# Optimization experiments

Measured on AMD Instinct MI355X. Metric: run time of the kernel, lower is better.

The kernel has to match this reference:

```python
import jax, jax.numpy as jnp
import numpy as np

B, C_FEAT, C_CODE, H, W = 32, 768, 70, 28, 28
FS = 11
NEG = 5
POS_INTRA_SHIFT = 0.18
POS_INTER_SHIFT = 0.12
NEG_INTER_SHIFT = 0.46


def _norm(t):
    # F.normalize(t, dim=1, eps=1e-10)
    n = jnp.sqrt(jnp.sum(t * t, axis=1, keepdims=True))
    return t / jnp.maximum(n, 1e-10)


def _grid_sample(t, coords):
    # torch: F.grid_sample(t, coords.permute(0,2,1,3), padding_mode='border', align_corners=True)
    grid = jnp.transpose(coords, (0, 2, 1, 3))  # [N, Hg, Wg, 2], last dim = (x, y)
    N, C, Hi, Wi = t.shape
    # align_corners=True unnormalize, then border-clip the continuous coordinate
    x = jnp.clip((grid[..., 0] + 1.0) * 0.5 * (Wi - 1), 0.0, Wi - 1.0)
    y = jnp.clip((grid[..., 1] + 1.0) * 0.5 * (Hi - 1), 0.0, Hi - 1.0)
    x0 = jnp.floor(x)
    y0 = jnp.floor(y)
    wx = (x - x0)[:, None]  # broadcast over channel dim
    wy = (y - y0)[:, None]
    x0i = x0.astype(jnp.int32)
    y0i = y0.astype(jnp.int32)
    x1i = jnp.minimum(x0i + 1, Wi - 1)
    y1i = jnp.minimum(y0i + 1, Hi - 1)
    gather = jax.vmap(lambda img, yi, xi: img[:, yi, xi])  # [C,Hg,Wg] per batch elem
    v00 = gather(t, y0i, x0i)
    v01 = gather(t, y0i, x1i)
    v10 = gather(t, y1i, x0i)
    v11 = gather(t, y1i, x1i)
    return (v00 * (1.0 - wx) * (1.0 - wy) + v01 * wx * (1.0 - wy)
            + v10 * (1.0 - wx) * wy + v11 * wx * wy)


def _helper(f1, f2, c1, c2, shift):
    # fd under torch.no_grad -> stop_gradient
    fd = jnp.einsum('nchw,ncij->nhwij', _norm(f1), _norm(f2))
    old_mean = fd.mean()  # pointwise=True branch
    fd = fd - fd.mean(axis=(3, 4), keepdims=True)
    fd = jax.lax.stop_gradient(fd - fd.mean() + old_mean)
    cd = jnp.einsum('nchw,ncij->nhwij', _norm(c1), _norm(c2))
    # zero_clamp=True -> min_val=0.0; stabalize=True -> clamp max 0.8
    loss = -jnp.clip(cd, 0.0, 0.8) * (fd - shift)
    return loss, cd


def _forward(orig_feats, orig_feats_pos, orig_code, orig_code_pos,
             depth_aug_feats, depth_aug_feats_pos, coords1, coords2, perms):
    c1 = coords1 * 2.0 - 1.0
    c2 = coords2 * 2.0 - 1.0
    feats = _grid_sample(orig_feats, c1)
    code = _grid_sample(orig_code, c1)
    feats_pos = _grid_sample(orig_feats_pos, c2)
    code_pos = _grid_sample(orig_code_pos, c2)
    daf = _grid_sample(depth_aug_feats, c1)
    _ = _grid_sample(depth_aug_feats_pos, c2)  # computed (as in torch) but unused

    pos_intra_loss, pos_intra_cd = _helper(daf, daf, code, code, POS_INTRA_SHIFT)
    pos_inter_loss, pos_inter_cd = _helper(feats, feats_pos, code, code_pos, POS_INTER_SHIFT)

    neg_losses, neg_cds = [], []
    for i in range(perms.shape[0]):  # fixed small neg_samples loop
        p = perms[i]
        feats_neg = _grid_sample(orig_feats[p], c2)
        code_neg = _grid_sample(orig_code[p], c2)
        l, cd = _helper(feats, feats_neg, code, code_neg, NEG_INTER_SHIFT)
        neg_losses.append(l)
        neg_cds.append(cd)
    neg_inter_loss = jnp.concatenate(neg_losses, axis=0)
    neg_inter_cd = jnp.concatenate(neg_cds, axis=0)
    return (pos_intra_loss.mean(), pos_intra_cd,
            pos_inter_loss.mean(), pos_inter_cd,
            neg_inter_loss, neg_inter_cd)


def setup_inputs() -> dict:
    key = jax.random.key(0)
    ks = jax.random.split(key, 10)
    rng = np.random.default_rng(0)
    perms = []
    for _ in range(NEG):  # super_perm: derangement-ish permutation
        p = rng.permutation(B)
        p = np.where(p == np.arange(B), p + 1, p) % B
        perms.append(p)
    return {
        'orig_feats': jax.random.normal(ks[0], (B, C_FEAT, H, W), jnp.float32),
        'orig_feats_pos': jax.random.normal(ks[1], (B, C_FEAT, H, W), jnp.float32),
        'orig_salience': jnp.zeros((B, H, W), jnp.float32),
        'orig_salience_pos': jnp.zeros((B, H, W), jnp.float32),
        'orig_code': jax.random.normal(ks[2], (B, C_CODE, H, W), jnp.float32),
        'orig_code_pos': jax.random.normal(ks[3], (B, C_CODE, H, W), jnp.float32),
        'depth_aug_feats': jax.random.normal(ks[4], (B, C_FEAT, H, W), jnp.float32),
        'depth_aug_feats_pos': jax.random.normal(ks[5], (B, C_FEAT, H, W), jnp.float32),
        'coords1': jax.random.uniform(ks[6], (B, FS, FS, 2), jnp.float32),
        'coords2': jax.random.uniform(ks[7], (B, FS, FS, 2), jnp.float32),
        'perms': jnp.asarray(np.stack(perms), dtype=jnp.int32),
    }


def reference(orig_feats, orig_feats_pos, orig_salience, orig_salience_pos,
              orig_code, orig_code_pos, depth_aug_feats, depth_aug_feats_pos,
              coords1, coords2, perms):
    # use_salience=False: salience tensors unused
    return _forward(orig_feats, orig_feats_pos, orig_code, orig_code_pos,
                    depth_aug_feats, depth_aug_feats_pos, coords1, coords2, perms)
```

## Files before the change

### kernel.cpp

```cpp
#include <hip/hip_runtime.h>

#define CF 768
#define CCODE 70
#define NPIX 784
#define P 121
#define NB 32
#define NTOTF 468512.0f

#define OFF_PI_SCALAR 0
#define OFF_PI_CD 1
#define OFF_PO_SCALAR 468513
#define OFF_PO_CD 468514
#define OFF_NEG_LOSS 937026
#define OFF_NEG_CD 3279586

#define WS_BSUMS 0
#define WS_ADDT 1536
#define WS_NSQF 2048
#define WS_NSQC 395264
#define WS_FRAG_FLOAT 423936
#define FEAT_FRAG_SHORTS 98304
#define CODE_FRAG_SHORTS 12288
#define FEATS_TOTAL_SHORTS (8 * 32 * FEAT_FRAG_SHORTS)
#define CODE_BASE_SHORTS FEATS_TOTAL_SHORTS
#define CODE_TOTAL_SHORTS (7 * 32 * CODE_FRAG_SHORTS)
#define WS_NEED2 (WS_FRAG_FLOAT + (FEATS_TOTAL_SHORTS + CODE_TOTAL_SHORTS) / 2)

typedef __attribute__((ext_vector_type(8))) short short8;
typedef __attribute__((ext_vector_type(4))) float f32x4;
typedef unsigned short ushort_t;
typedef unsigned int uint_t;

__device__ __forceinline__ float samp4(const float* __restrict__ img, int c,
                                       const int4 o, const float4 w) {
  const float* p = img + c * NPIX;
  return w.x * p[o.x] + w.y * p[o.y] + w.z * p[o.z] + w.w * p[o.w];
}

__device__ __forceinline__ void mkcoord(const float* cp, int4* o, float4* w) {
  float x = fminf(fmaxf(cp[0] * 27.f, 0.f), 27.f);
  float y = fminf(fmaxf(cp[1] * 27.f, 0.f), 27.f);
  float x0f = floorf(x), y0f = floorf(y);
  int x0 = (int)x0f, y0 = (int)y0f;
  int x1 = min(x0 + 1, 27), y1 = min(y0 + 1, 27);
  float wx = x - x0f, wy = y - y0f;
  *o = make_int4(y0 * 28 + x0, y0 * 28 + x1, y1 * 28 + x0, y1 * 28 + x1);
  *w = make_float4((1.f - wx) * (1.f - wy), wx * (1.f - wy),
                   (1.f - wx) * wy, wx * wy);
}

__device__ __forceinline__ void mkcoord2(const float* cp, int2* o, float4* w) {
  float x = fminf(fmaxf(cp[0] * 27.f, 0.f), 27.f);
  float y = fminf(fmaxf(cp[1] * 27.f, 0.f), 27.f);
  float x0f = floorf(x), y0f = floorf(y);
  int x0 = (int)x0f, y0 = (int)y0f;
  int y1 = min(y0 + 1, 27);
  float wx = x - x0f, wy = y - y0f;
  bool sh = (x0 >= 27);
  int xb = sh ? 26 : x0;
  float wa0 = sh ? 0.f : (1.f - wx) * (1.f - wy);
  float wa1 = sh ? (1.f - wy) : wx * (1.f - wy);
  float wb0 = sh ? 0.f : (1.f - wx) * wy;
  float wb1 = sh ? wy : wx * wy;
  *o = make_int2(y0 * 28 + xb, y1 * 28 + xb);
  *w = make_float4(wa0, wa1, wb0, wb1);
}

__device__ __forceinline__ ushort_t f2bf(float x) {
  uint_t u = __float_as_uint(x);
  u += 0x7fffu + ((u >> 16) & 1u);
  return (ushort_t)(u >> 16);
}

__global__ __launch_bounds__(256) void presample_fz(
    const float* __restrict__ OF, const float* __restrict__ OFP,
    const float* __restrict__ OC, const float* __restrict__ OCP,
    const float* __restrict__ DAF,
    const float* __restrict__ CO1, const float* __restrict__ CO2,
    const int* __restrict__ PERMS, float* __restrict__ ws) {
  ushort_t* frags = (ushort_t*)(ws + WS_FRAG_FLOAT);
  __shared__ float planes[8 * NPIX];
  __shared__ int sh_slot[16], sh_n[16], sh_cb[16];
  __shared__ int sh_ncs;
  const int job = (int)(((long long)blockIdx.x * 405) % 1216);
  const int tid = threadIdx.x;

  int tensor, m, g0, G;
  if (job < 384) { tensor = 0; m = job / 12; g0 = (job - m * 12) * 8; G = 8; }
  else if (job < 768) { int j = job - 384; tensor = 1; m = j / 12; g0 = (j - m * 12) * 8; G = 8; }
  else if (job < 1152) { int j = job - 768; tensor = 2; m = j / 12; g0 = (j - m * 12) * 8; G = 8; }
  else if (job < 1184) { tensor = 3; m = job - 1152; g0 = 0; G = 12; }
  else { tensor = 4; m = job - 1184; g0 = 0; G = 12; }

  const float* src;
  int nch;
  bool feat;
  if (tensor == 0) { src = OF + (size_t)m * CF * NPIX; nch = CF; feat = true; }
  else if (tensor == 1) { src = DAF + (size_t)m * CF * NPIX; nch = CF; feat = true; }
  else if (tensor == 2) { src = OFP + (size_t)m * CF * NPIX; nch = CF; feat = true; }
  else if (tensor == 3) { src = OC + (size_t)m * CCODE * NPIX; nch = CCODE; feat = false; }
  else { src = OCP + (size_t)m * CCODE * NPIX; nch = CCODE; feat = false; }

  if (tid == 0) {
    int cnt = 0;
    if (tensor == 0) {
      sh_slot[0] = 1; sh_n[0] = m; sh_cb[0] = 0; cnt = 1;
      for (int i = 0; i < 5; ++i)
        for (int k = 0; k < NB; ++k)
          if (PERMS[i * NB + k] == m) {
            sh_slot[cnt] = 3 + i; sh_n[cnt] = k; sh_cb[cnt] = 1; ++cnt;
          }
    } else if (tensor == 1) { sh_slot[0] = 0; sh_n[0] = m; sh_cb[0] = 0; cnt = 1; }
    else if (tensor == 2) { sh_slot[0] = 2; sh_n[0] = m; sh_cb[0] = 1; cnt = 1; }
    else if (tensor == 3) {
      sh_slot[0] = 0; sh_n[0] = m; sh_cb[0] = 0; cnt = 1;
      for (int i = 0; i < 5; ++i)
        for (int k = 0; k < NB; ++k)
          if (PERMS[i * NB + k] == m) {
            sh_slot[cnt] = 2 + i; sh_n[cnt] = k; sh_cb[cnt] = 1; ++cnt;
          }
    } else { sh_slot[0] = 1; sh_n[0] = m; sh_cb[0] = 1; cnt = 1; }
    sh_ncs = cnt;
  }

  float4 buf0, buf1, buf2, buf3, buf4, buf5, buf6;
#define LOAD_OCT(OCT)                                                        \
  {                                                                          \
    const int c0_ = (OCT) * 8;                                               \
    int valid_ = nch - c0_;                                                  \
    valid_ = valid_ > 8 ? 8 : (valid_ < 0 ? 0 : valid_);                     \
    const int lim4_ = valid_ * (NPIX / 4);                                   \
    const float4* sc_ = (const float4*)(src + (size_t)c0_ * NPIX);           \
    int e_;                                                                  \
    e_ = tid;          buf0 = (e_ < lim4_) ? sc_[e_] : make_float4(0,0,0,0); \
    e_ = tid + 256;    buf1 = (e_ < lim4_) ? sc_[e_] : make_float4(0,0,0,0); \
    e_ = tid + 512;    buf2 = (e_ < lim4_) ? sc_[e_] : make_float4(0,0,0,0); \
    e_ = tid + 768;    buf3 = (e_ < lim4_) ? sc_[e_] : make_float4(0,0,0,0); \
    e_ = tid + 1024;   buf4 = (e_ < lim4_) ? sc_[e_] : make_float4(0,0,0,0); \
    e_ = tid + 1280;   buf5 = (e_ < lim4_) ? sc_[e_] : make_float4(0,0,0,0); \
    e_ = tid + 1536;                                                         \
    buf6 = (e_ < 1568 && e_ < lim4_) ? sc_[e_] : make_float4(0,0,0,0);       \
  }

  LOAD_OCT(g0);
  __syncthreads();

  const int total = sh_ncs * 128;
  const int sub = g0 >> 3;
  int2 o_0, o_1, o_2, o_3, o_4, o_5;
  float4 w_0, w_1, w_2, w_3, w_4, w_5;
  uint_t b_0 = 0, b_1 = 0, b_2 = 0, b_3 = 0, b_4 = 0, b_5 = 0;
  uint_t nq_0 = 0, nq_1 = 0, nq_2 = 0, nq_3 = 0, nq_4 = 0, nq_5 = 0;
  float sq_0 = 0.f, sq_1 = 0.f, sq_2 = 0.f, sq_3 = 0.f, sq_4 = 0.f, sq_5 = 0.f;
#define SETUP_SLOT(J, OV, WV, BV, NQV)                                       \
  {                                                                          \
    const int s_ = tid + (J) * 256;                                          \
    OV = make_int2(0, 0);                                                    \
    WV = make_float4(0.f, 0.f, 0.f, 0.f);                                    \
    if (s_ < total) {                                                        \
      const int cs_ = s_ >> 7, pt_ = s_ & 127;                               \
      const int slot_ = sh_slot[cs_], n_ = sh_n[cs_];                        \
      const float* cb_ = sh_cb[cs_] ? CO2 : CO1;                             \
      size_t fb_ = feat ? (size_t)(slot_ * 32 + n_) * FEAT_FRAG_SHORTS       \
                        : CODE_BASE_SHORTS +                                 \
                              (size_t)(slot_ * 32 + n_) * CODE_FRAG_SHORTS;  \
      BV = (uint_t)(fb_ + ((size_t)((pt_ >> 4) * 64 + (pt_ & 15)) << 3));    \
      NQV = feat ? (uint_t)(WS_NSQF +                                        \
                            ((slot_ * 32 + n_) * 12 + sub) * 128 + pt_)      \
                 : (uint_t)(WS_NSQC + (slot_ * 32 + n_) * 128 + pt_);        \
      if (pt_ < P) {                                                         \
        int gi_ = pt_ / 11, gj_ = pt_ - gi_ * 11;                            \
        mkcoord2(cb_ + (((n_ * 11 + gj_) * 11 + gi_) << 1), &OV, &WV);       \
      }                                                                      \
    }                                                                        \
  }
  SETUP_SLOT(0, o_0, w_0, b_0, nq_0)
  SETUP_SLOT(1, o_1, w_1, b_1, nq_1)
  SETUP_SLOT(2, o_2, w_2, b_2, nq_2)
  SETUP_SLOT(3, o_3, w_3, b_3, nq_3)
  SETUP_SLOT(4, o_4, w_4, b_4, nq_4)
  SETUP_SLOT(5, o_5, w_5, b_5, nq_5)
#undef SETUP_SLOT

#define DO_SLOT(J, OV, WV, BV, SQV)                                          \
  if (tid + (J) * 256 < total) {                                             \
    float v_[8];                                                             \
    _Pragma("unroll") for (int i_ = 0; i_ < 8; ++i_) {                       \
      const float* pl_ = planes + i_ * NPIX;                                 \
      v_[i_] = WV.x * pl_[OV.x] + WV.y * pl_[OV.x + 1] +                     \
               WV.z * pl_[OV.y] + WV.w * pl_[OV.y + 1];                      \
      SQV = fmaf(v_[i_], v_[i_], SQV);                                       \
    }                                                                        \
    uint4 q_;                                                                \
    q_.x = (uint_t)f2bf(v_[0]) | ((uint_t)f2bf(v_[1]) << 16);                \
    q_.y = (uint_t)f2bf(v_[2]) | ((uint_t)f2bf(v_[3]) << 16);                \
    q_.z = (uint_t)f2bf(v_[4]) | ((uint_t)f2bf(v_[5]) << 16);                \
    q_.w = (uint_t)f2bf(v_[6]) | ((uint_t)f2bf(v_[7]) << 16);                \
    *(uint4*)(frags + BV + octoff) = q_;                                     \
  }

  for (int g = 0; g < G; ++g) {
    const int o = g0 + g;
    if (g) __syncthreads();
    {
      float4* pl4 = (float4*)planes;
      int e;
      e = tid;        pl4[e] = buf0;
      e = tid + 256;  pl4[e] = buf1;
      e = tid + 512;  pl4[e] = buf2;
      e = tid + 768;  pl4[e] = buf3;
      e = tid + 1024; pl4[e] = buf4;
      e = tid + 1280; pl4[e] = buf5;
      e = tid + 1536; if (e < 1568) pl4[e] = buf6;
    }
    __syncthreads();
    if (g + 1 < G) LOAD_OCT(g0 + g + 1);

    const uint_t octoff = (uint_t)((o >> 2) * 4096 + (o & 3) * 128);
    DO_SLOT(0, o_0, w_0, b_0, sq_0)
    DO_SLOT(1, o_1, w_1, b_1, sq_1)
    DO_SLOT(2, o_2, w_2, b_2, sq_2)
    DO_SLOT(3, o_3, w_3, b_3, sq_3)
    DO_SLOT(4, o_4, w_4, b_4, sq_4)
    DO_SLOT(5, o_5, w_5, b_5, sq_5)
  }
#undef DO_SLOT
#undef LOAD_OCT

  if (tid < total) ws[nq_0] = sq_0;
  if (tid + 256 < total) ws[nq_1] = sq_1;
  if (tid + 512 < total) ws[nq_2] = sq_2;
  if (tid + 768 < total) ws[nq_3] = sq_3;
  if (tid + 1024 < total) ws[nq_4] = sq_4;
  if (tid + 1280 < total) ws[nq_5] = sq_5;
}

__global__ __launch_bounds__(256) void gram_mfma2(float* __restrict__ ws,
                                                  float* __restrict__ out) {
  const ushort_t* frags = (const ushort_t*)(ws + WS_FRAG_FLOAT);
  const int bid = blockIdx.x;
  const int half = bid & 1, pairn = bid >> 1;
  const int pair = pairn >> 5, n = pairn & 31;
  const int tid = threadIdx.x, wave = tid >> 6, lane = tid & 63;
  __shared__ float invAf[128], invBf[128], invAc[128], invBc[128];
  __shared__ float red[4][3];
  const int afslot = (pair == 0) ? 0 : 1;
  const int bfslot = (pair == 0) ? 0 : (pair == 1 ? 2 : 3 + (pair - 2));
  const int bcslot = (pair == 0) ? 0 : (pair == 1 ? 1 : 2 + (pair - 2));
  if (tid < 128) {
    float s;
    const float* p;
    p = ws + WS_NSQF + (size_t)(afslot * 32 + n) * 12 * 128 + tid;
    s = 0.f;
#pragma unroll
    for (int u = 0; u < 12; ++u) s += p[u * 128];
    invAf[tid] = 1.f / fmaxf(sqrtf(s), 1e-10f);
    p = ws + WS_NSQF + (size_t)(bfslot * 32 + n) * 12 * 128 + tid;
    s = 0.f;
#pragma unroll
    for (int u = 0; u < 12; ++u) s += p[u * 128];
    invBf[tid] = 1.f / fmaxf(sqrtf(s), 1e-10f);
    invAc[tid] = 1.f / fmaxf(sqrtf(ws[WS_NSQC + (0 * 32 + n) * 128 + tid]), 1e-10f);
    invBc[tid] = 1.f / fmaxf(sqrtf(ws[WS_NSQC + (bcslot * 32 + n) * 128 + tid]), 1e-10f);
  }
  __syncthreads();

  const short8* Af = (const short8*)(frags + (size_t)(afslot * 32 + n) * FEAT_FRAG_SHORTS);
  const short8* Bf = (const short8*)(frags + (size_t)(bfslot * 32 + n) * FEAT_FRAG_SHORTS);
  const int rt = half * 4 + wave;

  f32x4 acc[8];
#pragma unroll
  for (int t = 0; t < 8; ++t) acc[t] = (f32x4){0.f, 0.f, 0.f, 0.f};

#pragma unroll 2
  for (int kp = 0; kp < 24; ++kp) {
    short8 a0 = Af[(kp * 8 + rt) * 64 + lane];
    short8 bv[8];
#pragma unroll
    for (int t = 0; t < 8; ++t) bv[t] = Bf[(kp * 8 + t) * 64 + lane];
#pragma unroll
    for (int t = 0; t < 8; ++t)
      acc[t] = __builtin_amdgcn_mfma_f32_16x16x32_bf16(a0, bv[t], acc[t], 0, 0, 0);
  }

  const int lane4 = (lane >> 4) << 2;
  const int cl15 = lane & 15;
  const int rb = rt * 16 + lane4;
  float sfd = 0.f;
  {
    const float ivr0 = invAf[rb], ivr1 = invAf[rb + 1], ivr2 = invAf[rb + 2],
                ivr3 = invAf[rb + 3];
    float rs0 = 0.f, rs1 = 0.f, rs2 = 0.f, rs3 = 0.f;
#pragma unroll
    for (int t = 0; t < 8; ++t) {
      const float ivc = invBf[t * 16 + cl15];
      float v0 = acc[t].x * ivr0 * ivc;
      float v1 = acc[t].y * ivr1 * ivc;
      float v2 = acc[t].z * ivr2 * ivc;
      float v3 = acc[t].w * ivr3 * ivc;
      acc[t].x = v0; acc[t].y = v1; acc[t].z = v2; acc[t].w = v3;
      rs0 += v0; rs1 += v1; rs2 += v2; rs3 += v3;
    }
    sfd = rs0 + rs1 + rs2 + rs3;
    rs0 += __shfl_xor(rs0, 1); rs0 += __shfl_xor(rs0, 2);
    rs0 += __shfl_xor(rs0, 4); rs0 += __shfl_xor(rs0, 8);
    rs1 += __shfl_xor(rs1, 1); rs1 += __shfl_xor(rs1, 2);
    rs1 += __shfl_xor(rs1, 4); rs1 += __shfl_xor(rs1, 8);
    rs2 += __shfl_xor(rs2, 1); rs2 += __shfl_xor(rs2, 2);
    rs2 += __shfl_xor(rs2, 4); rs2 += __shfl_xor(rs2, 8);
    rs3 += __shfl_xor(rs3, 1); rs3 += __shfl_xor(rs3, 2);
    rs3 += __shfl_xor(rs3, 4); rs3 += __shfl_xor(rs3, 8);
    const float rm0 = rs0 * (1.f / 121.f), rm1 = rs1 * (1.f / 121.f);
    const float rm2 = rs2 * (1.f / 121.f), rm3 = rs3 * (1.f / 121.f);
#pragma unroll
    for (int t = 0; t < 8; ++t) {
      acc[t].x -= rm0; acc[t].y -= rm1; acc[t].z -= rm2; acc[t].w -= rm3;
    }
  }

  int cd_base, loss_base = 0;
  if (pair == 0) cd_base = OFF_PI_CD + n * 14641;
  else if (pair == 1) cd_base = OFF_PO_CD + n * 14641;
  else {
    int t0 = ((pair - 2) * NB + n) * 14641;
    cd_base = OFF_NEG_CD + t0;
    loss_base = OFF_NEG_LOSS + t0;
  }

  if (pair >= 2 && rb < P) {
#pragma unroll
    for (int t = 0; t < 8; ++t) {
      const int c = t * 16 + cl15;
      if (c < P) {
        float* o = out + loss_base + rb * P + c;
        o[0] = acc[t].x;
        if (rb + 1 < P) o[P] = acc[t].y;
        if (rb + 2 < P) o[2 * P] = acc[t].z;
        if (rb + 3 < P) o[3 * P] = acc[t].w;
      }
    }
  }

  const short8* Ac = (const short8*)(frags + CODE_BASE_SHORTS + (size_t)n * CODE_FRAG_SHORTS);
  const short8* Bc = (const short8*)(frags + CODE_BASE_SHORTS + (size_t)(bcslot * 32 + n) * CODE_FRAG_SHORTS);
  f32x4 cacc[8];
#pragma unroll
  for (int t = 0; t < 8; ++t) cacc[t] = (f32x4){0.f, 0.f, 0.f, 0.f};
#pragma unroll
  for (int kp = 0; kp < 3; ++kp) {
    short8 a0 = Ac[(kp * 8 + rt) * 64 + lane];
    short8 bv[8];
#pragma unroll
    for (int t = 0; t < 8; ++t) bv[t] = Bc[(kp * 8 + t) * 64 + lane];
#pragma unroll
    for (int t = 0; t < 8; ++t)
      cacc[t] = __builtin_amdgcn_mfma_f32_16x16x32_bf16(a0, bv[t], cacc[t], 0, 0, 0);
  }

  float s1 = 0.f, s2 = 0.f;
  {
    const float ivr0 = invAc[rb], ivr1 = invAc[rb + 1], ivr2 = invAc[rb + 2],
                ivr3 = invAc[rb + 3];
#pragma unroll
    for (int t = 0; t < 8; ++t) {
      const int c = t * 16 + cl15;
      const float ivc = invBc[c];
      float c0v = cacc[t].x * ivr0 * ivc;
      float c1v = cacc[t].y * ivr1 * ivc;
      float c2v = cacc[t].z * ivr2 * ivc;
      float c3v = cacc[t].w * ivr3 * ivc;
      if (c < P && rb < P) {
        float* o = out + cd_base + rb * P + c;
        o[0] = c0v;
        if (rb + 1 < P) o[P] = c1v;
        if (rb + 2 < P) o[2 * P] = c2v;
        if (rb + 3 < P) o[3 * P] = c3v;
      }
      if (pair < 2) {
        float cl0 = fminf(fmaxf(c0v, 0.f), 0.8f);
        float cl1 = fminf(fmaxf(c1v, 0.f), 0.8f);
        float cl2 = fminf(fmaxf(c2v, 0.f), 0.8f);
        float cl3 = fminf(fmaxf(c3v, 0.f), 0.8f);
        s1 = fmaf(cl0, acc[t].x, s1);
        s1 = fmaf(cl1, acc[t].y, s1);
        s1 = fmaf(cl2, acc[t].z, s1);
        s1 = fmaf(cl3, acc[t].w, s1);
        s2 += cl0 + cl1 + cl2 + cl3;
      }
    }
  }

#pragma unroll
  for (int m = 1; m < 64; m <<= 1) {
    sfd += __shfl_xor(sfd, m);
    s1 += __shfl_xor(s1, m);
    s2 += __shfl_xor(s2, m);
  }
  if ((tid & 63) == 0) { red[wave][0] = sfd; red[wave][1] = s1; red[wave][2] = s2; }
  __syncthreads();
  if (tid == 0) {
    float a = 0.f, b2 = 0.f, c2 = 0.f;
    for (int w = 0; w < 4; ++w) { a += red[w][0]; b2 += red[w][1]; c2 += red[w][2]; }
    float* bsums = ws + WS_BSUMS;
    bsums[bid * 3 + 0] = a;
    bsums[bid * 3 + 1] = b2;
    bsums[bid * 3 + 2] = c2;
  }
}

__global__ void loss_finish3(float* __restrict__ ws, float* __restrict__ out) {
  __shared__ float s[7][3];
  const float* bsums = ws + WS_BSUMS;
  float* addterm = ws + WS_ADDT;
  int tid = threadIdx.x;
  if (tid < 21) {
    int pr = tid / 3, k = tid % 3;
    float a = 0.f;
    for (int i = 0; i < 64; ++i) a += bsums[(pr * 64 + i) * 3 + k];
    s[pr][k] = a;
  }
  __syncthreads();
  if (tid == 0) {
    const float invN = 1.f / NTOTF;
    out[OFF_PI_SCALAR] = -(s[0][1] + (s[0][0] * invN - 0.18f) * s[0][2]) * invN;
    out[OFF_PO_SCALAR] = -(s[1][1] + (s[1][0] * invN - 0.12f) * s[1][2]) * invN;
  }
  if (tid >= 1 && tid < 6) addterm[tid - 1] = s[tid + 1][0] / NTOTF - 0.46f;
}

__global__ __launch_bounds__(256) void neg_loss_kernel(
    float* __restrict__ lossr, const float* __restrict__ cdr,
    const float* __restrict__ addterm) {
  __shared__ float at[5];
  if (threadIdx.x < 5) at[threadIdx.x] = addterm[threadIdx.x];
  __syncthreads();
  const int total4 = 5 * 117128;
  float4* l4 = (float4*)lossr;
  const float4* c4 = (const float4*)cdr;
  for (int e = blockIdx.x * 256 + threadIdx.x; e < total4; e += gridDim.x * 256) {
    int k = e / 117128;
    float4 cd = c4[e];
    float4 fv = l4[e];
    float a = at[k];
    float4 r;
    r.x = -fminf(fmaxf(cd.x, 0.f), 0.8f) * (fv.x + a);
    r.y = -fminf(fmaxf(cd.y, 0.f), 0.8f) * (fv.y + a);
    r.z = -fminf(fmaxf(cd.z, 0.f), 0.8f) * (fv.z + a);
    r.w = -fminf(fmaxf(cd.w, 0.f), 0.8f) * (fv.w + a);
    l4[e] = r;
  }
}


__global__ __launch_bounds__(256) void loss_main_fb(
    const float* __restrict__ OF, const float* __restrict__ OFP,
    const float* __restrict__ OC, const float* __restrict__ OCP,
    const float* __restrict__ DAF,
    const float* __restrict__ CO1, const float* __restrict__ CO2,
    const int* __restrict__ PERMS,
    float* __restrict__ out, float* __restrict__ bsums) {
  const int b = blockIdx.x;
  const int pair = b >> 7;
  const int rem = b & 127;
  const int n = rem >> 2;
  const int rg = rem & 3;
  const int row_start = rg * 31;
  const int rcount = min(31, P - row_start);
  const int tid = threadIdx.x;
  const int tx = tid & 15, ty = tid >> 4;

  const float *F1, *F2, *C1, *C2, *CB;
  if (pair == 0) {
    F1 = DAF + (size_t)n * CF * NPIX; F2 = F1;
    C1 = OC + (size_t)n * CCODE * NPIX; C2 = C1;
    CB = CO1;
  } else if (pair == 1) {
    F1 = OF + (size_t)n * CF * NPIX; F2 = OFP + (size_t)n * CF * NPIX;
    C1 = OC + (size_t)n * CCODE * NPIX; C2 = OCP + (size_t)n * CCODE * NPIX;
    CB = CO2;
  } else {
    int n2 = PERMS[(pair - 2) * NB + n];
    F1 = OF + (size_t)n * CF * NPIX; F2 = OF + (size_t)n2 * CF * NPIX;
    C1 = OC + (size_t)n * CCODE * NPIX; C2 = OC + (size_t)n2 * CCODE * NPIX;
    CB = CO2;
  }

  __shared__ int4 Bo[P];
  __shared__ float4 Bw[P];
  __shared__ int4 Ao[32];
  __shared__ float4 Aw[32];
  __shared__ float Abuf[CCODE][32];
  __shared__ float Bbuf[CCODE][128];
  __shared__ float invA[32], invB[128];
  __shared__ float red[4][3];

  if (tid < P) {
    int gi = tid / 11, gj = tid - gi * 11;
    const float* cp = CB + (((n * 11 + gj) * 11 + gi) << 1);
    mkcoord(cp, &Bo[tid], &Bw[tid]);
  } else if (tid >= 128 && tid < 160) {
    int r = tid - 128;
    int q = row_start + r;
    if (q < P) {
      int gi = q / 11, gj = q - gi * 11;
      const float* cp = CO1 + (((n * 11 + gj) * 11 + gi) << 1);
      mkcoord(cp, &Ao[r], &Aw[r]);
    }
  }
  __syncthreads();

  float acc[2][2][4];
#pragma unroll
  for (int kr = 0; kr < 2; ++kr)
#pragma unroll
    for (int m = 0; m < 2; ++m)
#pragma unroll
      for (int u = 0; u < 4; ++u) acc[kr][m][u] = 0.f;
  float ansq = 0.f, bnsq = 0.f;

  for (int ch = 0; ch < 12; ++ch) {
    const int c0 = ch * 64;
    if (ch) __syncthreads();
    for (int e = tid; e < 64 * 128; e += 256) {
      int col = e & 127, cc = e >> 7;
      float v = 0.f;
      if (col < P) v = samp4(F2, c0 + cc, Bo[col], Bw[col]);
      Bbuf[cc][col] = v;
    }
    for (int e = tid; e < 64 * 32; e += 256) {
      int col = e & 31, cc = e >> 5;
      float v = 0.f;
      if (col < rcount) v = samp4(F1, c0 + cc, Ao[col], Aw[col]);
      Abuf[cc][col] = v;
    }
    __syncthreads();
    if (tid < 128) {
      float s = 0.f;
      for (int cc = 0; cc < 64; ++cc) { float v = Bbuf[cc][tid]; s = fmaf(v, v, s); }
      bnsq += s;
    } else if (tid < 160) {
      int r = tid - 128;
      float s = 0.f;
      for (int cc = 0; cc < 64; ++cc) { float v = Abuf[cc][r]; s = fmaf(v, v, s); }
      ansq += s;
    }
    for (int cc = 0; cc < 64; ++cc) {
      const float2 av = *(const float2*)&Abuf[cc][ty * 2];
      const float4 b0 = *(const float4*)&Bbuf[cc][tx * 4];
      const float4 b1 = *(const float4*)&Bbuf[cc][tx * 4 + 64];
      float a[2] = {av.x, av.y};
      float bb[2][4] = {{b0.x, b0.y, b0.z, b0.w}, {b1.x, b1.y, b1.z, b1.w}};
#pragma unroll
      for (int kr = 0; kr < 2; ++kr)
#pragma unroll
        for (int m = 0; m < 2; ++m)
#pragma unroll
          for (int u = 0; u < 4; ++u)
            acc[kr][m][u] = fmaf(a[kr], bb[m][u], acc[kr][m][u]);
    }
  }
  __syncthreads();
  if (tid < 128) invB[tid] = (tid < P) ? 1.f / fmaxf(sqrtf(bnsq), 1e-10f) : 0.f;
  else if (tid < 160) {
    int r = tid - 128;
    invA[r] = (r < rcount) ? 1.f / fmaxf(sqrtf(ansq), 1e-10f) : 0.f;
  }
  __syncthreads();

  float ia[2] = {invA[2 * ty], invA[2 * ty + 1]};
  float ib[2][4];
#pragma unroll
  for (int m = 0; m < 2; ++m)
#pragma unroll
    for (int u = 0; u < 4; ++u) ib[m][u] = invB[m * 64 + tx * 4 + u];

  float fdc[2][2][4];
  float sfd = 0.f;
#pragma unroll
  for (int kr = 0; kr < 2; ++kr) {
    float part = 0.f;
#pragma unroll
    for (int m = 0; m < 2; ++m)
#pragma unroll
      for (int u = 0; u < 4; ++u) {
        float v = acc[kr][m][u] * ia[kr] * ib[m][u];
        fdc[kr][m][u] = v;
        part += v;
      }
    sfd += part;
    float rs = part;
#pragma unroll
    for (int s = 1; s < 16; s <<= 1) rs += __shfl_xor(rs, s, 16);
    float rowm = rs * (1.f / 121.f);
#pragma unroll
    for (int m = 0; m < 2; ++m)
#pragma unroll
      for (int u = 0; u < 4; ++u) fdc[kr][m][u] -= rowm;
  }
  __syncthreads();

  for (int e = tid; e < CCODE * 128; e += 256) {
    int col = e & 127, cc = e >> 7;
    float v = 0.f;
    if (col < P) v = samp4(C2, cc, Bo[col], Bw[col]);
    Bbuf[cc][col] = v;
  }
  for (int e = tid; e < CCODE * 32; e += 256) {
    int col = e & 31, cc = e >> 5;
    float v = 0.f;
    if (col < rcount) v = samp4(C1, cc, Ao[col], Aw[col]);
    Abuf[cc][col] = v;
  }
  __syncthreads();
  if (tid < 128) {
    float s = 0.f;
    for (int cc = 0; cc < CCODE; ++cc) { float v = Bbuf[cc][tid]; s = fmaf(v, v, s); }
    invB[tid] = (tid < P) ? 1.f / fmaxf(sqrtf(s), 1e-10f) : 0.f;
  } else if (tid < 160) {
    int r = tid - 128;
    float s = 0.f;
    for (int cc = 0; cc < CCODE; ++cc) { float v = Abuf[cc][r]; s = fmaf(v, v, s); }
    invA[r] = (r < rcount) ? 1.f / fmaxf(sqrtf(s), 1e-10f) : 0.f;
  }
  float cacc[2][2][4];
#pragma unroll
  for (int kr = 0; kr < 2; ++kr)
#pragma unroll
    for (int m = 0; m < 2; ++m)
#pragma unroll
      for (int u = 0; u < 4; ++u) cacc[kr][m][u] = 0.f;
  for (int cc = 0; cc < CCODE; ++cc) {
    const float2 av = *(const float2*)&Abuf[cc][ty * 2];
    const float4 b0 = *(const float4*)&Bbuf[cc][tx * 4];
    const float4 b1 = *(const float4*)&Bbuf[cc][tx * 4 + 64];
    float a[2] = {av.x, av.y};
    float bb[2][4] = {{b0.x, b0.y, b0.z, b0.w}, {b1.x, b1.y, b1.z, b1.w}};
#pragma unroll
    for (int kr = 0; kr < 2; ++kr)
#pragma unroll
      for (int m = 0; m < 2; ++m)
#pragma unroll
        for (int u = 0; u < 4; ++u)
          cacc[kr][m][u] = fmaf(a[kr], bb[m][u], cacc[kr][m][u]);
  }
  __syncthreads();
  float iac[2] = {invA[2 * ty], invA[2 * ty + 1]};
  float ibc[2][4];
#pragma unroll
  for (int m = 0; m < 2; ++m)
#pragma unroll
    for (int u = 0; u < 4; ++u) ibc[m][u] = invB[m * 64 + tx * 4 + u];

  int cd_base, loss_base = 0;
  if (pair == 0) cd_base = OFF_PI_CD + n * 14641;
  else if (pair == 1) cd_base = OFF_PO_CD + n * 14641;
  else {
    int t = ((pair - 2) * NB + n) * 14641;
    cd_base = OFF_NEG_CD + t;
    loss_base = OFF_NEG_LOSS + t;
  }

  float s1 = 0.f, s2 = 0.f;
#pragma unroll
  for (int kr = 0; kr < 2; ++kr) {
    int r = 2 * ty + kr;
    if (r < rcount) {
      int rglob = row_start + r;
#pragma unroll
      for (int m = 0; m < 2; ++m)
#pragma unroll
        for (int u = 0; u < 4; ++u) {
          int c = m * 64 + tx * 4 + u;
          if (c < P) {
            float cdv = cacc[kr][m][u] * iac[kr] * ibc[m][u];
            int idx = rglob * P + c;
            out[cd_base + idx] = cdv;
            float cl = fminf(fmaxf(cdv, 0.f), 0.8f);
            float fv = fdc[kr][m][u];
            if (pair < 2) { s1 = fmaf(cl, fv, s1); s2 += cl; }
            else out[loss_base + idx] = fv;
          }
        }
    }
  }

#pragma unroll
  for (int s = 1; s < 64; s <<= 1) {
    sfd += __shfl_xor(sfd, s);
    s1 += __shfl_xor(s1, s);
    s2 += __shfl_xor(s2, s);
  }
  int wv = tid >> 6;
  if ((tid & 63) == 0) { red[wv][0] = sfd; red[wv][1] = s1; red[wv][2] = s2; }
  __syncthreads();
  if (tid == 0) {
    float a = 0.f, bb = 0.f, cc = 0.f;
    for (int w = 0; w < 4; ++w) { a += red[w][0]; bb += red[w][1]; cc += red[w][2]; }
    bsums[b * 3 + 0] = a;
    bsums[b * 3 + 1] = bb;
    bsums[b * 3 + 2] = cc;
  }
}

__global__ void loss_finish_fb(const float* __restrict__ bsums,
                               float* __restrict__ out,
                               float* __restrict__ addterm) {
  __shared__ float s[7][3];
  int tid = threadIdx.x;
  if (tid < 21) {
    int pr = tid / 3, k = tid % 3;
    float a = 0.f;
    const float* p = bsums + (pr * 128) * 3 + k;
    for (int i = 0; i < 128; ++i) a += p[i * 3];
    s[pr][k] = a;
  }
  __syncthreads();
  if (tid == 0) {
    const float invN = 1.f / NTOTF;
    out[OFF_PI_SCALAR] = -(s[0][1] + (s[0][0] * invN - 0.18f) * s[0][2]) * invN;
    out[OFF_PO_SCALAR] = -(s[1][1] + (s[1][0] * invN - 0.12f) * s[1][2]) * invN;
  }
  if (tid >= 1 && tid < 6) addterm[tid - 1] = s[tid + 1][0] / NTOTF - 0.46f;
}

__global__ __launch_bounds__(256) void neg_loss_fb(
    float* __restrict__ lossr, const float* __restrict__ cdr,
    const float* __restrict__ addterm) {
  __shared__ float at[5];
  if (threadIdx.x < 5) at[threadIdx.x] = addterm[threadIdx.x];
  __syncthreads();
  const int total = 5 * 468512;
  for (int e = blockIdx.x * 256 + threadIdx.x; e < total; e += gridDim.x * 256) {
    int k = e / 468512;
    float cdv = cdr[e];
    float cl = fminf(fmaxf(cdv, 0.f), 0.8f);
    lossr[e] = -cl * (lossr[e] + at[k]);
  }
}

extern "C" void kernel_launch(void* const* d_in, const int* in_sizes, int n_in,
                              void* d_out, int out_size, void* d_ws,
                              size_t ws_size, hipStream_t stream) {
  const float* OF = (const float*)d_in[0];
  const float* OFP = (const float*)d_in[1];
  const float* OC = (const float*)d_in[4];
  const float* OCP = (const float*)d_in[5];
  const float* DAF = (const float*)d_in[6];
  const float* CO1 = (const float*)d_in[8];
  const float* CO2 = (const float*)d_in[9];
  const int* PERMS = (const int*)d_in[10];
  float* out = (float*)d_out;
  float* ws = (float*)d_ws;

  if (ws_size >= (size_t)WS_NEED2 * sizeof(float)) {
    hipLaunchKernelGGL(presample_fz, dim3(1216), dim3(256), 0, stream,
                       OF, OFP, OC, OCP, DAF, CO1, CO2, PERMS, ws);
    hipLaunchKernelGGL(gram_mfma2, dim3(448), dim3(256), 0, stream, ws, out);
    hipLaunchKernelGGL(loss_finish3, dim3(1), dim3(64), 0, stream, ws, out);
    hipLaunchKernelGGL(neg_loss_kernel, dim3(2048), dim3(256), 0, stream,
                       out + OFF_NEG_LOSS, out + OFF_NEG_CD, ws + WS_ADDT);
  } else {
    float* bsums = ws;
    float* addterm = bsums + 896 * 3;
    hipLaunchKernelGGL(loss_main_fb, dim3(896), dim3(256), 0, stream,
                       OF, OFP, OC, OCP, DAF, CO1, CO2, PERMS, out, bsums);
    hipLaunchKernelGGL(loss_finish_fb, dim3(1), dim3(64), 0, stream,
                       bsums, out, addterm);
    hipLaunchKernelGGL(neg_loss_fb, dim3(2048), dim3(256), 0, stream,
                       out + OFF_NEG_LOSS, out + OFF_NEG_CD, addterm);
  }
}
```

Baseline: 139.7 us.

## Stage presample feature planes into double-buffered LDS via direct global-to-LDS loads

Replaces the register-staged prefetch of each 8-channel plane group with __builtin_amdgcn_global_load_lds direct-to-LDS copies into two ping-pong LDS buffers. Each iteration issues the next group's load into the other buffer while sampling from the current one, which drops the register buffers and one barrier per iteration. LDS use doubles to about 50KB per block, which may reduce occupancy. There is also a correctness risk: no explicit wait on the async LDS loads (vmcnt) is visible before the barrier.

```diff
diff --git a/kernel.cpp b/kernel.cpp
--- a/kernel.cpp
+++ b/kernel.cpp
@@ -72,18 +72,20 @@
   return (ushort_t)(u >> 16);
 }
 
-__global__ __launch_bounds__(256) void presample_fz(
+__global__ __launch_bounds__(256) void presample_dma(
     const float* __restrict__ OF, const float* __restrict__ OFP,
     const float* __restrict__ OC, const float* __restrict__ OCP,
     const float* __restrict__ DAF,
     const float* __restrict__ CO1, const float* __restrict__ CO2,
     const int* __restrict__ PERMS, float* __restrict__ ws) {
   ushort_t* frags = (ushort_t*)(ws + WS_FRAG_FLOAT);
-  __shared__ float planes[8 * NPIX];
+  __shared__ float planes0[8 * NPIX];
+  __shared__ float planes1[8 * NPIX];
   __shared__ int sh_slot[16], sh_n[16], sh_cb[16];
   __shared__ int sh_ncs;
   const int job = (int)(((long long)blockIdx.x * 405) % 1216);
   const int tid = threadIdx.x;
+  const int wv64 = tid >> 6;
 
   int tensor, m, g0, G;
   if (job < 384) { tensor = 0; m = job / 12; g0 = (job - m * 12) * 8; G = 8; }
@@ -100,6 +102,41 @@
   else if (tensor == 2) { src = OFP + (size_t)m * CF * NPIX; nch = CF; feat = true; }
   else if (tensor == 3) { src = OC + (size_t)m * CCODE * NPIX; nch = CCODE; feat = false; }
   else { src = OCP + (size_t)m * CCODE * NPIX; nch = CCODE; feat = false; }
+
+#define STAGE(OCT, PL)                                                        \
+  {                                                                           \
+    const int c0_ = (OCT) * 8;                                                \
+    const float4* sc_ = (const float4*)(src + (size_t)c0_ * NPIX);            \
+    float4* pb_ = (float4*)(PL);                                              \
+    if (c0_ + 8 <= nch) {                                                     \
+      _Pragma("unroll") for (int k_ = 0; k_ < 6; ++k_) {                      \
+        __builtin_amdgcn_global_load_lds(                                     \
+            (const __attribute__((address_space(1))) uint_t*)(const void*)    \
+                (sc_ + k_ * 256 + tid),                                       \
+            (__attribute__((address_space(3))) uint_t*)(void*)                \
+                (pb_ + k_ * 256 + wv64 * 64),                                 \
+            16, 0, 0);                                                        \
+      }                                                                       \
+      if (tid < 32) {                                                         \
+        __builtin_amdgcn_global_load_lds(                                     \
+            (const __attribute__((address_space(1))) uint_t*)(const void*)    \
+                (sc_ + 1536 + tid),                                           \
+            (__attribute__((address_space(3))) uint_t*)(void*)(pb_ + 1536),   \
+            16, 0, 0);                                                        \
+      }                                                                       \
+    } else {                                                                  \
+      int valid_ = nch - c0_;                                                 \
+      valid_ = valid_ > 8 ? 8 : (valid_ < 0 ? 0 : valid_);                    \
+      const int lim4_ = valid_ * (NPIX / 4);                                  \
+      _Pragma("unroll") for (int k_ = 0; k_ < 7; ++k_) {                      \
+        const int e_ = tid + k_ * 256;                                        \
+        if (e_ < 1568)                                                        \
+          pb_[e_] = (e_ < lim4_) ? sc_[e_] : make_float4(0.f, 0.f, 0.f, 0.f); \
+      }                                                                       \
+    }                                                                         \
+  }
+
+  STAGE(g0, planes0);
 
   if (tid == 0) {
     int cnt = 0;
@@ -122,27 +159,6 @@
     } else { sh_slot[0] = 1; sh_n[0] = m; sh_cb[0] = 1; cnt = 1; }
     sh_ncs = cnt;
   }
-
-  float4 buf0, buf1, buf2, buf3, buf4, buf5, buf6;
-#define LOAD_OCT(OCT)                                                        \
-  {                                                                          \
-    const int c0_ = (OCT) * 8;                                               \
-    int valid_ = nch - c0_;                                                  \
-    valid_ = valid_ > 8 ? 8 : (valid_ < 0 ? 0 : valid_);                     \
-    const int lim4_ = valid_ * (NPIX / 4);                                   \
-    const float4* sc_ = (const float4*)(src + (size_t)c0_ * NPIX);           \
-    int e_;                                                                  \
-    e_ = tid;          buf0 = (e_ < lim4_) ? sc_[e_] : make_float4(0,0,0,0); \
-    e_ = tid + 256;    buf1 = (e_ < lim4_) ? sc_[e_] : make_float4(0,0,0,0); \
-    e_ = tid + 512;    buf2 = (e_ < lim4_) ? sc_[e_] : make_float4(0,0,0,0); \
-    e_ = tid + 768;    buf3 = (e_ < lim4_) ? sc_[e_] : make_float4(0,0,0,0); \
-    e_ = tid + 1024;   buf4 = (e_ < lim4_) ? sc_[e_] : make_float4(0,0,0,0); \
-    e_ = tid + 1280;   buf5 = (e_ < lim4_) ? sc_[e_] : make_float4(0,0,0,0); \
-    e_ = tid + 1536;                                                         \
-    buf6 = (e_ < 1568 && e_ < lim4_) ? sc_[e_] : make_float4(0,0,0,0);       \
-  }
-
-  LOAD_OCT(g0);
   __syncthreads();
 
   const int total = sh_ncs * 128;
@@ -186,7 +202,7 @@
   if (tid + (J) * 256 < total) {                                             \
     float v_[8];                                                             \
     _Pragma("unroll") for (int i_ = 0; i_ < 8; ++i_) {                       \
-      const float* pl_ = planes + i_ * NPIX;                                 \
+      const float* pl_ = PL + i_ * NPIX;                                     \
       v_[i_] = WV.x * pl_[OV.x] + WV.y * pl_[OV.x + 1] +                     \
                WV.z * pl_[OV.y] + WV.w * pl_[OV.y + 1];                      \
       SQV = fmaf(v_[i_], v_[i_], SQV);                                       \
@@ -201,20 +217,9 @@
 
   for (int g = 0; g < G; ++g) {
     const int o = g0 + g;
-    if (g) __syncthreads();
-    {
-      float4* pl4 = (float4*)planes;
-      int e;
-      e = tid;        pl4[e] = buf0;
-      e = tid + 256;  pl4[e] = buf1;
-      e = tid + 512;  pl4[e] = buf2;
-      e = tid + 768;  pl4[e] = buf3;
-      e = tid + 1024; pl4[e] = buf4;
-      e = tid + 1280; pl4[e] = buf5;
-      e = tid + 1536; if (e < 1568) pl4[e] = buf6;
-    }
-    __syncthreads();
-    if (g + 1 < G) LOAD_OCT(g0 + g + 1);
+    const float* PL = (g & 1) ? planes1 : planes0;
+    float* PN = (g & 1) ? planes0 : planes1;
+    if (g + 1 < G) STAGE(g0 + g + 1, PN);
 
     const uint_t octoff = (uint_t)((o >> 2) * 4096 + (o & 3) * 128);
     DO_SLOT(0, o_0, w_0, b_0, sq_0)
@@ -223,9 +228,10 @@
     DO_SLOT(3, o_3, w_3, b_3, sq_3)
     DO_SLOT(4, o_4, w_4, b_4, sq_4)
     DO_SLOT(5, o_5, w_5, b_5, sq_5)
+    __syncthreads();
   }
 #undef DO_SLOT
-#undef LOAD_OCT
+#undef STAGE
 
   if (tid < total) ws[nq_0] = sq_0;
   if (tid + 256 < total) ws[nq_1] = sq_1;
@@ -754,7 +760,7 @@
   float* ws = (float*)d_ws;
 
   if (ws_size >= (size_t)WS_NEED2 * sizeof(float)) {
-    hipLaunchKernelGGL(presample_fz, dim3(1216), dim3(256), 0, stream,
+    hipLaunchKernelGGL(presample_dma, dim3(1216), dim3(256), 0, stream,
                        OF, OFP, OC, OCP, DAF, CO1, CO2, PERMS, ws);
     hipLaunchKernelGGL(gram_mfma2, dim3(448), dim3(256), 0, stream, ws, out);
     hipLaunchKernelGGL(loss_finish3, dim3(1), dim3(64), 0, stream, ws, out);
```

After: 137.9 us (median of 2 runs). Within noise of the previous version (-1.3%).
